# Kernel optimization log

Hardware: AMD Instinct MI355X
Metric: run time of the kernel (lower is better)

## Reference

```python
import jax, jax.numpy as jnp
import numpy as np

TRIANGLE_TABLE = np.array([
    [-1,-1,-1,-1,-1,-1],[1,0,2,-1,-1,-1],[4,0,3,-1,-1,-1],[1,4,2,1,3,4],
    [3,1,5,-1,-1,-1],[2,3,0,2,5,3],[1,4,0,1,5,4],[4,2,5,-1,-1,-1],
    [4,5,2,-1,-1,-1],[4,1,0,4,5,1],[3,2,0,3,5,2],[1,3,5,-1,-1,-1],
    [4,1,2,4,3,1],[3,0,4,-1,-1,-1],[2,0,1,-1,-1,-1],[-1,-1,-1,-1,-1,-1]], dtype=np.int32)
NUM_TRI_TABLE = np.array([0,1,1,2,1,2,2,1,1,2,2,1,2,1,1,0], dtype=np.int32)
BASE_TET_EDGES = np.array([0,1,0,2,0,3,1,2,1,3,2,3], dtype=np.int32)

NV = 200_000
NT = 800_000

def setup_inputs() -> dict:
    key = jax.random.key(0)
    k1, k2, k3 = jax.random.split(key, 3)
    pos_nx3 = jax.random.normal(k1, (NV, 3), dtype=jnp.float32)
    sdf_n = jax.random.normal(k2, (NV,), dtype=jnp.float32)
    tet_fx4 = jax.random.randint(k3, (NT, 4), 0, NV, dtype=jnp.int32)
    return {"pos_nx3": pos_nx3, "sdf_n": sdf_n, "tet_fx4": tet_fx4}

def map_uv(face_gidx, max_idx):
    # Faithful port of DMTet.map_uv: one 2-triangle UV quad per (potential) tet.
    N = int(np.ceil(np.sqrt((max_idx + 1) // 2)))
    lin = jnp.linspace(0.0, 1.0 - 1.0 / N, N, dtype=jnp.float32)
    tex_y, tex_x = jnp.meshgrid(lin, lin, indexing='ij')
    pad = 0.9 / N
    uvs = jnp.stack([tex_x, tex_y, tex_x + pad, tex_y,
                     tex_x + pad, tex_y + pad, tex_x, tex_y + pad], axis=-1).reshape(-1, 2)
    t = face_gidx // 2
    tet_idx = (t // N) * N + (t % N)   # identity for t < N*N, kept faithful
    tri_idx = face_gidx % 2
    uv_idx = jnp.stack([tet_idx * 4, tet_idx * 4 + tri_idx + 1, tet_idx * 4 + tri_idx + 2], axis=-1)
    return uvs, uv_idx.reshape(-1, 3)

def reference(pos_nx3, sdf_n, tet_fx4):
    # NOTE: marching-tets output sizes are data dependent -> eager (non-jit) jax,
    # matching the torch.unique / boolean-mask structure of the original.
    tri_table = jnp.asarray(TRIANGLE_TABLE)
    num_tri_table = jnp.asarray(NUM_TRI_TABLE)
    base_edges = jnp.asarray(BASE_TET_EDGES)

    occ_n = sdf_n > 0                                   # [Nv]
    occ_fx4 = occ_n[tet_fx4]                            # [T,4]
    occ_sum = occ_fx4.sum(-1)
    valid_tets = (occ_sum > 0) & (occ_sum < 4)

    tet_valid = tet_fx4[valid_tets]                     # [Tv,4]
    all_edges = tet_valid[:, base_edges].reshape(-1, 2) # [Tv*6,2]
    all_edges = jnp.sort(all_edges, axis=1)             # == sort_edges
    unique_edges, idx_map = jnp.unique(all_edges, axis=0, return_inverse=True)

    mask_edges = occ_n[unique_edges].sum(-1) == 1       # sign-crossing edges
    mapping = jnp.where(mask_edges, jnp.cumsum(mask_edges) - 1, -1)
    idx_map = mapping[idx_map.reshape(-1)].reshape(-1, 6)
    interp_v = unique_edges[mask_edges]                 # [Ne,2]

    # linear interpolation of crossing point along each edge
    p = pos_nx3[interp_v]                               # [Ne,2,3]
    s = sdf_n[interp_v] * jnp.array([1.0, -1.0], dtype=sdf_n.dtype)  # negate 2nd sdf
    denom = s.sum(1, keepdims=True)                     # [Ne,1]
    w = s[:, ::-1] / denom                              # flip + normalize
    verts = (p * w[:, :, None]).sum(1)                  # [Ne,3]

    v_id = jnp.array([1, 2, 4, 8], dtype=jnp.int32)
    tetindex = (occ_fx4[valid_tets].astype(jnp.int32) * v_id).sum(-1)  # [Tv]
    num_triangles = num_tri_table[tetindex]
    m1 = num_triangles == 1
    m2 = num_triangles == 2
    f1 = jnp.take_along_axis(idx_map[m1], tri_table[tetindex[m1]][:, :3], axis=1).reshape(-1, 3)
    f2 = jnp.take_along_axis(idx_map[m2], tri_table[tetindex[m2]][:, :6], axis=1).reshape(-1, 3)
    faces = jnp.concatenate([f1, f2], axis=0)

    num_tets = tet_fx4.shape[0]
    tet_gidx = jnp.arange(num_tets, dtype=jnp.int32)[valid_tets]
    face_gidx = jnp.concatenate([
        tet_gidx[m1] * 2,
        jnp.stack([tet_gidx[m2] * 2, tet_gidx[m2] * 2 + 1], axis=-1).reshape(-1)], axis=0)

    uvs, uv_idx = map_uv(face_gidx, num_tets * 2)
    return verts, faces, uvs, uv_idx
```

## Files before the change

kernel.cpp:

```cpp
#include <hip/hip_runtime.h>
#include <cstdio>
#include <cstdint>

typedef unsigned long long u64;

static const int kNV = 200000;
static const int kNT = 800000;
static const int kNUV = 895;
#define UVS_ROWS   3204100LL
#define UVS_FLOATS 6408200LL
#define CAP 3300000

#define NH 392
#define TILE_T 2048
#define BINW 32
#define BSH 5
#define NBIN 6250
#define SUBSH 15
#define FINEB 256
#define MAXBIN 1536
#define C 6

__device__ const int c_tri[16][6] = {
    {-1,-1,-1,-1,-1,-1},{1,0,2,-1,-1,-1},{4,0,3,-1,-1,-1},{1,4,2,1,3,4},
    {3,1,5,-1,-1,-1},{2,3,0,2,5,3},{1,4,0,1,5,4},{4,2,5,-1,-1,-1},
    {4,5,2,-1,-1,-1},{4,1,0,4,5,1},{3,2,0,3,5,2},{1,3,5,-1,-1,-1},
    {4,1,2,4,3,1},{3,0,4,-1,-1,-1},{2,0,1,-1,-1,-1},{-1,-1,-1,-1,-1,-1}};
__device__ const int c_ntri[16]   = {0,1,1,2,1,2,2,1,1,2,2,1,2,1,1,0};
__device__ const int c_ncross[16] = {0,3,3,4,3,4,4,3,3,4,4,3,4,3,3,0};
__device__ const int c_edges[12] = {0,1,0,2,0,3,1,2,1,3,2,3};

#define PK(m1,m2,nc) (((u64)(m1) << 44) | ((u64)(m2) << 24) | (u64)(nc))

__device__ __forceinline__ int blockScanExcl(int v, volatile int* wsum, int tid, int* totalOut){
  int lane = tid & 63, wv = tid >> 6;
  int x = v;
  #pragma unroll
  for (int off = 1; off < 64; off <<= 1){
    int t = __shfl_up(x, off, 64);
    if (lane >= off) x += t;
  }
  __syncthreads();
  if (lane == 63) wsum[wv] = x;
  __syncthreads();
  int carry = 0;
  #pragma unroll
  for (int w = 0; w < 4; w++) if (w < wv) carry += wsum[w];
  if (totalOut) *totalOut = wsum[0] + wsum[1] + wsum[2] + wsum[3];
  return carry + x - v;
}

#define SCAN_B 256
#define SCAN_I 8
#define SCAN_TILE (SCAN_B*SCAN_I)

template<typename T>
__global__ void k_scan_partial(const T* __restrict__ in, T* __restrict__ partials, int n){
  __shared__ T sm[SCAN_B];
  int b = blockIdx.x;
  long long base = (long long)b*SCAN_TILE;
  T sum = 0;
  for (int i = threadIdx.x; i < SCAN_TILE; i += SCAN_B){
    long long idx = base + i;
    if (idx < n) sum += in[idx];
  }
  sm[threadIdx.x] = sum; __syncthreads();
  for (int s = SCAN_B/2; s > 0; s >>= 1){
    if ((int)threadIdx.x < s) sm[threadIdx.x] += sm[threadIdx.x + s];
    __syncthreads();
  }
  if (threadIdx.x == 0) partials[b] = sm[0];
}

template<typename T>
__global__ void k_scan_blocksums(T* __restrict__ partials, int nb, T* __restrict__ total_out){
  __shared__ T sm[SCAN_B];
  T carry = 0;
  for (int base = 0; base < nb; base += SCAN_B){
    int i = base + (int)threadIdx.x;
    T v = (i < nb) ? partials[i] : (T)0;
    sm[threadIdx.x] = v; __syncthreads();
    for (int off = 1; off < SCAN_B; off <<= 1){
      T t = ((int)threadIdx.x >= off) ? sm[threadIdx.x - off] : (T)0;
      __syncthreads();
      sm[threadIdx.x] += t;
      __syncthreads();
    }
    if (i < nb) partials[i] = carry + sm[threadIdx.x] - v;
    T tilesum = sm[SCAN_B-1];
    __syncthreads();
    carry += tilesum;
  }
  if (threadIdx.x == 0 && total_out) *total_out = carry;
}

template<typename T>
__global__ void k_scan_apply(const T* __restrict__ in, T* __restrict__ out,
                             const T* __restrict__ partials, int n){
  __shared__ T sm[SCAN_B];
  int b = blockIdx.x;
  long long base = (long long)b*SCAN_TILE + (long long)threadIdx.x*SCAN_I;
  T v[SCAN_I]; T s = 0;
  #pragma unroll
  for (int k = 0; k < SCAN_I; k++){ long long idx = base + k; v[k] = (idx < n) ? in[idx] : (T)0; s += v[k]; }
  sm[threadIdx.x] = s; __syncthreads();
  for (int off = 1; off < 256; off <<= 1){
    T t = ((int)threadIdx.x >= off) ? sm[threadIdx.x - off] : (T)0;
    __syncthreads();
    sm[threadIdx.x] += t;
    __syncthreads();
  }
  T excl = sm[threadIdx.x] - s + partials[b];
  #pragma unroll
  for (int k = 0; k < SCAN_I; k++){ long long idx = base + k; if (idx < n) out[idx] = excl; excl += v[k]; }
}

template<typename T>
static void run_scan(const T* in, T* out, int n, T* partials, hipStream_t s){
  int nb = (n + SCAN_TILE - 1) / SCAN_TILE;
  k_scan_partial<T><<<nb, SCAN_B, 0, s>>>(in, partials, n);
  k_scan_blocksums<T><<<1, SCAN_B, 0, s>>>(partials, nb, out + n);
  k_scan_apply<T><<<nb, SCAN_B, 0, s>>>(in, out, partials, n);
}


__global__ void k_classify_hist(const int* __restrict__ tet, const float* __restrict__ sdf,
                                int* __restrict__ tetinfo, u64* __restrict__ pk,
                                int* __restrict__ blockHist, u64* __restrict__ pkPart){
  __shared__ int h[NBIN];
  __shared__ u64 red[256];
  int blk = blockIdx.x;
  for (int j = threadIdx.x; j < NBIN; j += 256) h[j] = 0;
  __syncthreads();
  int t0 = blk*TILE_T;
  u64 myPk = 0;
  for (int k = 0; k < TILE_T/256; k++){
    int t = t0 + k*256 + threadIdx.x;
    if (t < kNT){
      int4 v4 = ((const int4*)tet)[t];
      int pat = ((sdf[v4.x] > 0.0f) ? 1 : 0) | ((sdf[v4.y] > 0.0f) ? 2 : 0)
              | ((sdf[v4.z] > 0.0f) ? 4 : 0) | ((sdf[v4.w] > 0.0f) ? 8 : 0);
      tetinfo[t] = pat;
      int nt_ = c_ntri[pat];
      u64 pv = PK(nt_ == 1, nt_ == 2, c_ncross[pat]);
      pk[t] = pv;
      myPk += pv;
      if (pat != 0 && pat != 15){
        int vv[4] = {v4.x, v4.y, v4.z, v4.w};
        #pragma unroll
        for (int e = 0; e < 6; e++){
          int i0 = c_edges[2*e], i1 = c_edges[2*e+1];
          if (((pat >> i0) & 1) != ((pat >> i1) & 1)){
            int a = vv[i0], b = vv[i1]; if (a > b){ int tm = a; a = b; b = tm; }
            atomicAdd(&h[a >> BSH], 1);
          }
        }
      }
    }
  }
  red[threadIdx.x] = myPk;
  __syncthreads();
  for (int s = 128; s > 0; s >>= 1){
    if ((int)threadIdx.x < s) red[threadIdx.x] += red[threadIdx.x + s];
    __syncthreads();
  }
  if (threadIdx.x == 0) pkPart[blk] = red[0];
  for (int j = threadIdx.x; j < NBIN; j += 256) blockHist[j*NH + blk] = h[j];
}

__global__ void k_scatter(const int* __restrict__ tet, const int* __restrict__ tetinfo,
                          const u64* __restrict__ psum, const int* __restrict__ bhScan,
                          u64* __restrict__ ebin){
  __shared__ int c[NBIN];
  int blk = blockIdx.x;
  for (int j = threadIdx.x; j < NBIN; j += 256) c[j] = bhScan[j*NH + blk];
  __syncthreads();
  int t0 = blk*TILE_T;
  for (int k = 0; k < TILE_T/256; k++){
    int t = t0 + k*256 + threadIdx.x;
    if (t < kNT){
      int pat = tetinfo[t];
      if (pat != 0 && pat != 15){
        int4 v4 = ((const int4*)tet)[t];
        int vv[4] = {v4.x, v4.y, v4.z, v4.w};
        int seq = (int)(psum[t] & 0xFFFFFF);
        #pragma unroll
        for (int e = 0; e < 6; e++){
          int i0 = c_edges[2*e], i1 = c_edges[2*e+1];
          if (((pat >> i0) & 1) != ((pat >> i1) & 1)){
            int a = vv[i0], b = vv[i1]; if (a > b){ int tm = a; a = b; b = tm; }
            int pos = atomicAdd(&c[a >> BSH], 1);
            ebin[pos] = ((u64)(unsigned)a << 40) | ((u64)(unsigned)b << 22) | (unsigned)seq;
            seq++;
          }
        }
      }
    }
  }
}

__global__ void k_fineflags(const int* __restrict__ bhScan, const u64* __restrict__ ebin,
                            unsigned* __restrict__ metaBySeq, u64* __restrict__ vfirst,
                            int* __restrict__ binFirstCnt){
  __shared__ u64 ld[MAXBIN];
  __shared__ unsigned char fl[MAXBIN];
  __shared__ unsigned short fp[MAXBIN];
  __shared__ int h[FINEB];
  __shared__ int wsum[4];
  int bin = blockIdx.x, tid = threadIdx.x;
  int binStart = bhScan[bin*NH];
  int binEnd   = bhScan[(bin+1)*NH];
  int n = binEnd - binStart;
  int a0 = bin << BSH;
  for (int j = tid; j < FINEB; j += 256) h[j] = 0;
  __syncthreads();
  if (n <= MAXBIN){
    u64 pr[C]; int kr[C];
    #pragma unroll
    for (int k = 0; k < C; k++){
      int i = tid + k*256;
      if (i < n){
        u64 p = ebin[binStart + i];
        pr[k] = p;
        kr[k] = (((int)(p >> 40) - a0) << 3) | ((int)((p >> 22) & 0x3FFFF) >> SUBSH);
      } else kr[k] = -1;
    }
    #pragma unroll
    for (int k = 0; k < C; k++) if (kr[k] >= 0) atomicAdd(&h[kr[k]], 1);
    __syncthreads();
    int s0 = h[tid];
    int excl = blockScanExcl(s0, wsum, tid, nullptr);
    h[tid] = excl;
    __syncthreads();
    #pragma unroll
    for (int k = 0; k < C; k++)
      if (kr[k] >= 0) ld[atomicAdd(&h[kr[k]], 1)] = pr[k];
    __syncthreads();
    #pragma unroll
    for (int k = 0; k < C; k++){
      int x = tid + k*256;
      if (x < n){
        u64 my = ld[x] >> 22;
        int key = (((int)(my >> 18) - a0) << 3) | ((int)(my & 0x3FFFF) >> SUBSH);
        int gs = key ? h[key-1] : 0;
        unsigned char f = 1;
        for (int y = x-1; y >= gs; y--){ if ((ld[y] >> 22) == my){ f = 0; break; } }
        fl[x] = f;
      } else if (x < MAXBIN) fl[x] = 0;
    }
    __syncthreads();
    int cbase = tid*C;
    int loc[C]; int cs = 0;
    #pragma unroll
    for (int q = 0; q < C; q++){ loc[q] = fl[cbase+q]; cs += loc[q]; }
    int tot;
    int ex2 = blockScanExcl(cs, wsum, tid, &tot);
    #pragma unroll
    for (int q = 0; q < C; q++){ fp[cbase+q] = (unsigned short)ex2; ex2 += loc[q]; }
    if (tid == 0) binFirstCnt[bin] = tot;
    __syncthreads();
    #pragma unroll
    for (int k = 0; k < C; k++){
      int x = tid + k*256;
      if (x < n){
        u64 p = ld[x];
        u64 my = p >> 22;
        int key = (((int)(my >> 18) - a0) << 3) | ((int)(my & 0x3FFFF) >> SUBSH);
        int gs = key ? h[key-1] : 0;
        int ge = h[key];
        int rk = 0;
        for (int y = gs; y < ge; y++){ if (fl[y] && (ld[y] >> 22) < my) rk++; }
        int rp = (int)fp[gs] + rk;
        metaBySeq[(int)(p & 0x3FFFFF)] = ((unsigned)bin << 12) | (unsigned)rp;
        if (fl[x]) vfirst[binStart + rp] = p;
      }
    }
  } else {
    if (tid == 0){
      int fcnt = 0;
      for (int x = 0; x < n; x++){
        u64 px = ebin[binStart+x];
        u64 kx = px >> 22;
        int f = 1;
        for (int y = 0; y < x; y++) if ((ebin[binStart+y] >> 22) == kx){ f = 0; break; }
        int rp = 0;
        for (int y = 0; y < n; y++){
          u64 ky = ebin[binStart+y] >> 22;
          if (ky < kx){
            int fy = 1;
            for (int z = 0; z < y; z++) if ((ebin[binStart+z] >> 22) == ky){ fy = 0; break; }
            rp += fy;
          }
        }
        if (f){ vfirst[binStart + rp] = px; fcnt++; }
        metaBySeq[(int)(px & 0x3FFFFF)] = ((unsigned)bin << 12) | (unsigned)rp;
      }
      binFirstCnt[bin] = fcnt;
    }
  }
}

__global__ void k_verts(const int* __restrict__ bhScan, const u64* __restrict__ vfirst,
                        const int* __restrict__ binPref, const float* __restrict__ pos,
                        const float* __restrict__ sdf, float* __restrict__ out){
  int bin = blockIdx.x;
  int binStart = bhScan[bin*NH];
  int rbase = binPref[bin];
  int cnt = binPref[bin+1] - rbase;
  for (int f = threadIdx.x; f < cnt; f += 256){
    u64 p = vfirst[binStart + f];
    int a = (int)(p >> 40);
    int b = (int)((p >> 22) & 0x3FFFF);
    float sa = sdf[a], sb = sdf[b];
    float denom = sa - sb;
    float w0 = (-sb) / denom;
    float w1 = sa / denom;
    long long r = rbase + f;
    out[3*r + 0] = pos[3*a+0]*w0 + pos[3*b+0]*w1;
    out[3*r + 1] = pos[3*a+1]*w0 + pos[3*b+1]*w1;
    out[3*r + 2] = pos[3*a+2]*w0 + pos[3*b+2]*w1;
  }
}

__global__ void k_faces(const int* __restrict__ tetinfo, const u64* __restrict__ psum,
                        const int* __restrict__ binPref, const unsigned* __restrict__ metaBySeq,
                        float* __restrict__ out){
  int t = blockIdx.x*256 + threadIdx.x; if (t >= kNT) return;
  int pat = tetinfo[t];
  int nt_ = c_ntri[pat];
  if (nt_ == 0) return;
  u64 tot = psum[kNT];
  int Nm1 = (int)(tot >> 44), Nm2 = (int)((tot >> 24) & 0xFFFFF);
  int Ne = binPref[NBIN];
  long long faces_off = 3LL*Ne;
  long long uvidx_off = faces_off + 3LL*((long long)Nm1 + 2LL*Nm2) + UVS_FLOATS;
  u64 ps = psum[t];
  int m1v = (int)(ps >> 44), m2v = (int)((ps >> 24) & 0xFFFFF);
  int seq = (int)(ps & 0xFFFFFF);
  int er[6];
  int j = 0;
  #pragma unroll
  for (int e = 0; e < 6; e++){
    int i0 = c_edges[2*e], i1 = c_edges[2*e+1];
    if (((pat >> i0) & 1) != ((pat >> i1) & 1)){
      unsigned m = metaBySeq[seq + j];
      er[e] = binPref[m >> 12] + (int)(m & 0xFFF);
      j++;
    } else er[e] = -1;
  }
  for (int k = 0; k < nt_; k++){
    long long row = (nt_ == 1) ? (long long)m1v : ((long long)Nm1 + 2LL*m2v + k);
    #pragma unroll
    for (int c = 0; c < 3; c++){
      int slot = c_tri[pat][3*k + c];
      out[faces_off + 3*row + c] = (float)er[slot];
    }
    out[uvidx_off + 3*row + 0] = (float)(4*t);
    out[uvidx_off + 3*row + 1] = (float)(4*t + k + 1);
    out[uvidx_off + 3*row + 2] = (float)(4*t + k + 2);
  }
}

__global__ void k_uvs(const u64* __restrict__ psum, const int* __restrict__ binPref,
                      float* __restrict__ out){
  long long r = (long long)blockIdx.x*256 + threadIdx.x;
  if (r >= UVS_ROWS) return;
  u64 tot = psum[kNT];
  int Nm1 = (int)(tot >> 44), Nm2 = (int)((tot >> 24) & 0xFFFFF);
  int Ne = binPref[NBIN];
  long long off = 3LL*Ne + 3LL*((long long)Nm1 + 2LL*Nm2);
  int cell = (int)(r >> 2), k = (int)(r & 3);
  int iy = cell / kNUV, ix = cell - iy*kNUV;
  const float delta = (1.0f - 1.0f/895.0f) / 894.0f;
  const float pad = 0.9f / 895.0f;
  float x = (float)ix * delta, y = (float)iy * delta;
  float u = x + ((k == 1 || k == 2) ? pad : 0.0f);
  float v = y + ((k >= 2) ? pad : 0.0f);
  if ((off & 1) == 0){
    float2 uv = make_float2(u, v);
    *reinterpret_cast<float2*>(&out[off + 2*r]) = uv;
  } else {
    out[off + 2*r]     = u;
    out[off + 2*r + 1] = v;
  }
}

static inline int divup(int a, int b){ return (a + b - 1) / b; }

extern "C" void kernel_launch(void* const* d_in, const int* in_sizes, int n_in,
                              void* d_out, int out_size, void* d_ws, size_t ws_size,
                              hipStream_t stream){
  const float* pos = (const float*)d_in[0];
  const float* sdf = (const float*)d_in[1];
  const int*   tet = (const int*)d_in[2];
  float* out = (float*)d_out;

  char* ws = (char*)d_ws;
  size_t off = 0;
  auto alloc = [&](size_t bytes) -> char* {
    char* p = ws + off; off += (bytes + 255) & ~(size_t)255; return p;
  };
  int* tetinfo      = (int*)alloc((size_t)kNT*4);
  u64* pk           = (u64*)alloc((size_t)kNT*8);
  u64* psum         = (u64*)alloc((size_t)(kNT+1)*8);
  int* blockHist    = (int*)alloc((size_t)NBIN*NH*4);
  int* bhScan       = (int*)alloc((size_t)(NBIN*NH+1)*4);
  u64* ebin         = (u64*)alloc((size_t)CAP*8);
  u64* vfirst       = (u64*)alloc((size_t)CAP*8);
  unsigned* metaBySeq = (unsigned*)alloc((size_t)CAP*4);
  int* binFirstCnt  = (int*)alloc((size_t)(NBIN+1)*4);
  u64* pkPart       = (u64*)alloc((size_t)NH*8);
  int* partI        = (int*)alloc(4096*4);
  if (off > ws_size){
    fprintf(stderr, "[dmtet] workspace too small: need %zu have %zu\n", off, ws_size);
    return;
  }

  k_classify_hist<<<NH, 256, 0, stream>>>(tet, sdf, tetinfo, pk, blockHist, pkPart);
  k_scan_blocksums<u64><<<1, SCAN_B, 0, stream>>>(pkPart, NH, psum + kNT);
  k_scan_apply<u64><<<divup(kNT,SCAN_TILE), SCAN_B, 0, stream>>>(pk, psum, pkPart, kNT);
  run_scan<int>(blockHist, bhScan, NBIN*NH, partI, stream);
  k_scatter<<<NH, 256, 0, stream>>>(tet, tetinfo, psum, bhScan, ebin);
  k_fineflags<<<NBIN, 256, 0, stream>>>(bhScan, ebin, metaBySeq, vfirst, binFirstCnt);
  k_scan_blocksums<int><<<1, SCAN_B, 0, stream>>>(binFirstCnt, NBIN, binFirstCnt + NBIN);
  k_verts<<<NBIN, 256, 0, stream>>>(bhScan, vfirst, binFirstCnt, pos, sdf, out);
  k_faces<<<divup(kNT,256), 256, 0, stream>>>(tetinfo, psum, binFirstCnt, metaBySeq, out);
  k_uvs<<<divup((int)UVS_ROWS,256), 256, 0, stream>>>(psum, binFirstCnt, out);
}
```

Baseline: 236.0 us.

## Replace full histogram scan with u16 column scan and recompute pk in scan

The per-tet pk array is no longer stored; the scan-apply kernel recomputes each tet's packed count from tetinfo and the lookup tables. The block histogram is written row-major as 16-bit counts and scanned per bin column by a simple serial kernel, followed by a small scan over the bin totals. This replaces the three-kernel scan over about 2.45M ints. The aim is to cut global memory traffic and kernel launches. The trade-off is a column scan where each of 6250 threads walks 392 rows serially with low parallelism, plus 16-bit counts that could overflow if one block's bin exceeds 65535.

After: 232.0 us. Within noise of the previous version (-1.7%).

```diff
diff --git a/kernel.cpp b/kernel.cpp
--- a/kernel.cpp
+++ b/kernel.cpp
@@ -3,6 +3,7 @@
 #include <cstdint>
 
 typedef unsigned long long u64;
+typedef unsigned short u16;
 
 static const int kNV = 200000;
 static const int kNT = 800000;
@@ -53,24 +54,6 @@
 #define SCAN_B 256
 #define SCAN_I 8
 #define SCAN_TILE (SCAN_B*SCAN_I)
-
-template<typename T>
-__global__ void k_scan_partial(const T* __restrict__ in, T* __restrict__ partials, int n){
-  __shared__ T sm[SCAN_B];
-  int b = blockIdx.x;
-  long long base = (long long)b*SCAN_TILE;
-  T sum = 0;
-  for (int i = threadIdx.x; i < SCAN_TILE; i += SCAN_B){
-    long long idx = base + i;
-    if (idx < n) sum += in[idx];
-  }
-  sm[threadIdx.x] = sum; __syncthreads();
-  for (int s = SCAN_B/2; s > 0; s >>= 1){
-    if ((int)threadIdx.x < s) sm[threadIdx.x] += sm[threadIdx.x + s];
-    __syncthreads();
-  }
-  if (threadIdx.x == 0) partials[b] = sm[0];
-}
 
 template<typename T>
 __global__ void k_scan_blocksums(T* __restrict__ partials, int nb, T* __restrict__ total_out){
@@ -94,39 +77,38 @@
   if (threadIdx.x == 0 && total_out) *total_out = carry;
 }
 
-template<typename T>
-__global__ void k_scan_apply(const T* __restrict__ in, T* __restrict__ out,
-                             const T* __restrict__ partials, int n){
-  __shared__ T sm[SCAN_B];
+__global__ void k_scan_apply_pk(const int* __restrict__ tetinfo, u64* __restrict__ out,
+                                const u64* __restrict__ partials){
+  __shared__ u64 sm[SCAN_B];
   int b = blockIdx.x;
   long long base = (long long)b*SCAN_TILE + (long long)threadIdx.x*SCAN_I;
-  T v[SCAN_I]; T s = 0;
+  u64 v[SCAN_I]; u64 s = 0;
   #pragma unroll
-  for (int k = 0; k < SCAN_I; k++){ long long idx = base + k; v[k] = (idx < n) ? in[idx] : (T)0; s += v[k]; }
+  for (int k = 0; k < SCAN_I; k++){
+    long long idx = base + k;
+    if (idx < kNT){
+      int pat = tetinfo[idx];
+      int nt_ = c_ntri[pat];
+      v[k] = PK(nt_ == 1, nt_ == 2, c_ncross[pat]);
+    } else v[k] = 0;
+    s += v[k];
+  }
   sm[threadIdx.x] = s; __syncthreads();
   for (int off = 1; off < 256; off <<= 1){
-    T t = ((int)threadIdx.x >= off) ? sm[threadIdx.x - off] : (T)0;
+    u64 t = ((int)threadIdx.x >= off) ? sm[threadIdx.x - off] : (u64)0;
     __syncthreads();
     sm[threadIdx.x] += t;
     __syncthreads();
   }
-  T excl = sm[threadIdx.x] - s + partials[b];
+  u64 excl = sm[threadIdx.x] - s + partials[b];
   #pragma unroll
-  for (int k = 0; k < SCAN_I; k++){ long long idx = base + k; if (idx < n) out[idx] = excl; excl += v[k]; }
-}
-
-template<typename T>
-static void run_scan(const T* in, T* out, int n, T* partials, hipStream_t s){
-  int nb = (n + SCAN_TILE - 1) / SCAN_TILE;
-  k_scan_partial<T><<<nb, SCAN_B, 0, s>>>(in, partials, n);
-  k_scan_blocksums<T><<<1, SCAN_B, 0, s>>>(partials, nb, out + n);
-  k_scan_apply<T><<<nb, SCAN_B, 0, s>>>(in, out, partials, n);
+  for (int k = 0; k < SCAN_I; k++){ long long idx = base + k; if (idx < kNT) out[idx] = excl; excl += v[k]; }
 }
 
 
 __global__ void k_classify_hist(const int* __restrict__ tet, const float* __restrict__ sdf,
-                                int* __restrict__ tetinfo, u64* __restrict__ pk,
-                                int* __restrict__ blockHist, u64* __restrict__ pkPart){
+                                int* __restrict__ tetinfo, u16* __restrict__ bh16,
+                                u64* __restrict__ pkPart){
   __shared__ int h[NBIN];
   __shared__ u64 red[256];
   int blk = blockIdx.x;
@@ -142,9 +124,7 @@
               | ((sdf[v4.z] > 0.0f) ? 4 : 0) | ((sdf[v4.w] > 0.0f) ? 8 : 0);
       tetinfo[t] = pat;
       int nt_ = c_ntri[pat];
-      u64 pv = PK(nt_ == 1, nt_ == 2, c_ncross[pat]);
-      pk[t] = pv;
-      myPk += pv;
+      myPk += PK(nt_ == 1, nt_ == 2, c_ncross[pat]);
       if (pat != 0 && pat != 15){
         int vv[4] = {v4.x, v4.y, v4.z, v4.w};
         #pragma unroll
@@ -165,15 +145,31 @@
     __syncthreads();
   }
   if (threadIdx.x == 0) pkPart[blk] = red[0];
-  for (int j = threadIdx.x; j < NBIN; j += 256) blockHist[j*NH + blk] = h[j];
+  for (int j = threadIdx.x; j < NBIN; j += 256)
+    bh16[(size_t)blk*NBIN + j] = (u16)h[j];
+}
+
+__global__ void k_colscan(const u16* __restrict__ bh16, int* __restrict__ rowScan,
+                          int* __restrict__ binStart){
+  int j = blockIdx.x*256 + threadIdx.x;
+  if (j >= NBIN) return;
+  int run = 0;
+  for (int blk = 0; blk < NH; blk++){
+    size_t idx = (size_t)blk*NBIN + j;
+    int v = bh16[idx];
+    rowScan[idx] = run;
+    run += v;
+  }
+  binStart[j] = run;
 }
 
 __global__ void k_scatter(const int* __restrict__ tet, const int* __restrict__ tetinfo,
-                          const u64* __restrict__ psum, const int* __restrict__ bhScan,
-                          u64* __restrict__ ebin){
+                          const u64* __restrict__ psum, const int* __restrict__ binStart,
+                          const int* __restrict__ rowScan, u64* __restrict__ ebin){
   __shared__ int c[NBIN];
   int blk = blockIdx.x;
-  for (int j = threadIdx.x; j < NBIN; j += 256) c[j] = bhScan[j*NH + blk];
+  for (int j = threadIdx.x; j < NBIN; j += 256)
+    c[j] = binStart[j] + rowScan[(size_t)blk*NBIN + j];
   __syncthreads();
   int t0 = blk*TILE_T;
   for (int k = 0; k < TILE_T/256; k++){
@@ -199,18 +195,18 @@
   }
 }
 
-__global__ void k_fineflags(const int* __restrict__ bhScan, const u64* __restrict__ ebin,
+__global__ void k_fineflags(const int* __restrict__ binStart, const u64* __restrict__ ebin,
                             unsigned* __restrict__ metaBySeq, u64* __restrict__ vfirst,
                             int* __restrict__ binFirstCnt){
   __shared__ u64 ld[MAXBIN];
   __shared__ unsigned char fl[MAXBIN];
-  __shared__ unsigned short fp[MAXBIN];
+  __shared__ u16 fp[MAXBIN];
   __shared__ int h[FINEB];
   __shared__ int wsum[4];
   int bin = blockIdx.x, tid = threadIdx.x;
-  int binStart = bhScan[bin*NH];
-  int binEnd   = bhScan[(bin+1)*NH];
-  int n = binEnd - binStart;
+  int bs = binStart[bin];
+  int be = binStart[bin+1];
+  int n = be - bs;
   int a0 = bin << BSH;
   for (int j = tid; j < FINEB; j += 256) h[j] = 0;
   __syncthreads();
@@ -220,7 +216,7 @@
     for (int k = 0; k < C; k++){
       int i = tid + k*256;
       if (i < n){
-        u64 p = ebin[binStart + i];
+        u64 p = ebin[bs + i];
         pr[k] = p;
         kr[k] = (((int)(p >> 40) - a0) << 3) | ((int)((p >> 22) & 0x3FFFF) >> SUBSH);
       } else kr[k] = -1;
@@ -256,7 +252,7 @@
     int tot;
     int ex2 = blockScanExcl(cs, wsum, tid, &tot);
     #pragma unroll
-    for (int q = 0; q < C; q++){ fp[cbase+q] = (unsigned short)ex2; ex2 += loc[q]; }
+    for (int q = 0; q < C; q++){ fp[cbase+q] = (u16)ex2; ex2 += loc[q]; }
     if (tid == 0) binFirstCnt[bin] = tot;
     __syncthreads();
     #pragma unroll
@@ -272,27 +268,27 @@
         for (int y = gs; y < ge; y++){ if (fl[y] && (ld[y] >> 22) < my) rk++; }
         int rp = (int)fp[gs] + rk;
         metaBySeq[(int)(p & 0x3FFFFF)] = ((unsigned)bin << 12) | (unsigned)rp;
-        if (fl[x]) vfirst[binStart + rp] = p;
+        if (fl[x]) vfirst[bs + rp] = p;
       }
     }
   } else {
     if (tid == 0){
       int fcnt = 0;
       for (int x = 0; x < n; x++){
-        u64 px = ebin[binStart+x];
+        u64 px = ebin[bs+x];
         u64 kx = px >> 22;
         int f = 1;
-        for (int y = 0; y < x; y++) if ((ebin[binStart+y] >> 22) == kx){ f = 0; break; }
+        for (int y = 0; y < x; y++) if ((ebin[bs+y] >> 22) == kx){ f = 0; break; }
         int rp = 0;
         for (int y = 0; y < n; y++){
-          u64 ky = ebin[binStart+y] >> 22;
+          u64 ky = ebin[bs+y] >> 22;
           if (ky < kx){
             int fy = 1;
-            for (int z = 0; z < y; z++) if ((ebin[binStart+z] >> 22) == ky){ fy = 0; break; }
+            for (int z = 0; z < y; z++) if ((ebin[bs+z] >> 22) == ky){ fy = 0; break; }
             rp += fy;
           }
         }
-        if (f){ vfirst[binStart + rp] = px; fcnt++; }
+        if (f){ vfirst[bs + rp] = px; fcnt++; }
         metaBySeq[(int)(px & 0x3FFFFF)] = ((unsigned)bin << 12) | (unsigned)rp;
       }
       binFirstCnt[bin] = fcnt;
@@ -300,15 +296,15 @@
   }
 }
 
-__global__ void k_verts(const int* __restrict__ bhScan, const u64* __restrict__ vfirst,
+__global__ void k_verts(const int* __restrict__ binStart, const u64* __restrict__ vfirst,
                         const int* __restrict__ binPref, const float* __restrict__ pos,
                         const float* __restrict__ sdf, float* __restrict__ out){
   int bin = blockIdx.x;
-  int binStart = bhScan[bin*NH];
+  int bs = binStart[bin];
   int rbase = binPref[bin];
   int cnt = binPref[bin+1] - rbase;
   for (int f = threadIdx.x; f < cnt; f += 256){
-    u64 p = vfirst[binStart + f];
+    u64 p = vfirst[bs + f];
     int a = (int)(p >> 40);
     int b = (int)((p >> 22) & 0x3FFFF);
     float sa = sdf[a], sb = sdf[b];
@@ -401,29 +397,29 @@
     char* p = ws + off; off += (bytes + 255) & ~(size_t)255; return p;
   };
   int* tetinfo      = (int*)alloc((size_t)kNT*4);
-  u64* pk           = (u64*)alloc((size_t)kNT*8);
   u64* psum         = (u64*)alloc((size_t)(kNT+1)*8);
-  int* blockHist    = (int*)alloc((size_t)NBIN*NH*4);
-  int* bhScan       = (int*)alloc((size_t)(NBIN*NH+1)*4);
+  u16* bh16         = (u16*)alloc((size_t)NH*NBIN*2);
+  int* rowScan      = (int*)alloc((size_t)NH*NBIN*4);
+  int* binStart     = (int*)alloc((size_t)(NBIN+1)*4);
   u64* ebin         = (u64*)alloc((size_t)CAP*8);
   u64* vfirst       = (u64*)alloc((size_t)CAP*8);
   unsigned* metaBySeq = (unsigned*)alloc((size_t)CAP*4);
   int* binFirstCnt  = (int*)alloc((size_t)(NBIN+1)*4);
   u64* pkPart       = (u64*)alloc((size_t)NH*8);
-  int* partI        = (int*)alloc(4096*4);
   if (off > ws_size){
     fprintf(stderr, "[dmtet] workspace too small: need %zu have %zu\n", off, ws_size);
     return;
   }
 
-  k_classify_hist<<<NH, 256, 0, stream>>>(tet, sdf, tetinfo, pk, blockHist, pkPart);
+  k_classify_hist<<<NH, 256, 0, stream>>>(tet, sdf, tetinfo, bh16, pkPart);
   k_scan_blocksums<u64><<<1, SCAN_B, 0, stream>>>(pkPart, NH, psum + kNT);
-  k_scan_apply<u64><<<divup(kNT,SCAN_TILE), SCAN_B, 0, stream>>>(pk, psum, pkPart, kNT);
-  run_scan<int>(blockHist, bhScan, NBIN*NH, partI, stream);
-  k_scatter<<<NH, 256, 0, stream>>>(tet, tetinfo, psum, bhScan, ebin);
-  k_fineflags<<<NBIN, 256, 0, stream>>>(bhScan, ebin, metaBySeq, vfirst, binFirstCnt);
+  k_scan_apply_pk<<<divup(kNT,SCAN_TILE), SCAN_B, 0, stream>>>(tetinfo, psum, pkPart);
+  k_colscan<<<divup(NBIN,256), 256, 0, stream>>>(bh16, rowScan, binStart);
+  k_scan_blocksums<int><<<1, SCAN_B, 0, stream>>>(binStart, NBIN, binStart + NBIN);
+  k_scatter<<<NH, 256, 0, stream>>>(tet, tetinfo, psum, binStart, rowScan, ebin);
+  k_fineflags<<<NBIN, 256, 0, stream>>>(binStart, ebin, metaBySeq, vfirst, binFirstCnt);
   k_scan_blocksums<int><<<1, SCAN_B, 0, stream>>>(binFirstCnt, NBIN, binFirstCnt + NBIN);
-  k_verts<<<NBIN, 256, 0, stream>>>(bhScan, vfirst, binFirstCnt, pos, sdf, out);
+  k_verts<<<NBIN, 256, 0, stream>>>(binStart, vfirst, binFirstCnt, pos, sdf, out);
   k_faces<<<divup(kNT,256), 256, 0, stream>>>(tetinfo, psum, binFirstCnt, metaBySeq, out);
   k_uvs<<<divup((int)UVS_ROWS,256), 256, 0, stream>>>(psum, binFirstCnt, out);
 }
```
